# Optimization experiments

Measured on AMD Instinct MI355X. Metric: run time of the kernel, lower is better.

Reference implementation:

```python
import jax, jax.numpy as jnp
import numpy as np

N_ENT = 50000
N_REL = 500
N_EDGE = 800000
H_DIM = 96
BN_EPS = 1e-5


def setup_inputs() -> dict:
    key = jax.random.key(0)
    k1, k2, k3, k4, k5 = jax.random.split(key, 5)
    return {
        "ent_emb": jax.random.normal(k1, (N_ENT, H_DIM), dtype=jnp.float32),
        "rel_emb": jax.random.normal(k2, (N_REL, H_DIM), dtype=jnp.float32),
        "neigh_w": jax.random.normal(k3, (H_DIM, H_DIM), dtype=jnp.float32) * (1.0 / np.sqrt(H_DIM)),
        "bn_gamma": jnp.ones((H_DIM,), dtype=jnp.float32),
        "bn_beta": jnp.zeros((H_DIM,), dtype=jnp.float32),
        "rel_id": jax.random.randint(k4, (N_EDGE,), 0, N_REL, dtype=jnp.int64),
        "dst": jax.random.randint(k5, (N_EDGE,), 0, N_ENT, dtype=jnp.int64),
    }


def reference(ent_emb, rel_emb, neigh_w, bn_gamma, bn_beta, rel_id, dst):
    n_nodes = ent_emb.shape[0]
    # per-edge gather: edge feature = relation embedding  [E, D]
    e = rel_emb[rel_id]
    # e_dot_v: dot of edge feature with destination node embedding  [E]
    score = jnp.sum(e * ent_emb[dst], axis=-1)
    # edge softmax over incoming edges of each destination node
    seg_max = jax.ops.segment_max(score, dst, num_segments=n_nodes)  # [N]
    w = jnp.exp(score - seg_max[dst])                                # [E]
    seg_sum = jax.ops.segment_sum(w, dst, num_segments=n_nodes)      # [N]
    alpha = w / seg_sum[dst]                                         # [E]
    # weighted scatter-sum aggregation into destination nodes  [N, D]
    neigh = jax.ops.segment_sum(e * alpha[:, None], dst, num_segments=n_nodes)
    # linear
    out = neigh @ neigh_w
    # BatchNorm1d (training mode: batch stats over nodes, biased var)
    mu = jnp.mean(out, axis=0)
    var = jnp.mean((out - mu) ** 2, axis=0)
    out = (out - mu) * jax.lax.rsqrt(var + BN_EPS) * bn_gamma + bn_beta
    return jnp.tanh(out)
```

## Files before the change

### kernel.cpp

```cpp
#include <hip/hip_runtime.h>
#include <math.h>

#define N_ENT   50000
#define N_REL   500
#define N_EDGE  800000
#define H       96
#define BN_EPS  1e-5f
#define DEG_CAP 48

#define BUCKET_BLOCKS ((N_EDGE + 255) / 256)
#define RELW_BLOCKS   ((N_REL * H + 255) / 256)

__global__ __launch_bounds__(256) void k_bucket_relw(
        const int* __restrict__ dst, const int* __restrict__ rel_id,
        int* __restrict__ cursor, unsigned short* __restrict__ pay,
        const float* __restrict__ rel, const float* __restrict__ W,
        float* __restrict__ relW) {
    if (blockIdx.x < BUCKET_BLOCKS) {
        int e = blockIdx.x * 256 + threadIdx.x;
        if (e >= N_EDGE) return;
        int d = dst[e];
        int r = rel_id[e];
        int p = atomicAdd(cursor + d, 1);
        if (p < DEG_CAP) pay[d * DEG_CAP + p] = (unsigned short)r;
    } else {
        int t = (blockIdx.x - BUCKET_BLOCKS) * 256 + threadIdx.x;
        if (t >= N_REL * H) return;
        int r = t / H;
        int c = t - r * H;
        const float* rr = rel + (size_t)r * H;
        const float* wc = W + c;
        float acc = 0.0f;
#pragma unroll 4
        for (int k = 0; k < H; ++k)
            acc += rr[k] * wc[(size_t)k * H];
        relW[t] = acc;
    }
}

__global__ __launch_bounds__(256) void k_node(
        const float* __restrict__ ent, const float* __restrict__ rel,
        const unsigned short* __restrict__ pay, const int* __restrict__ cursor,
        const float* __restrict__ relW, float* __restrict__ out) {
    __shared__ float sh_w[4][DEG_CAP];
    __shared__ int   sh_r[4][DEG_CAP];
    int wv   = threadIdx.x >> 6;
    int lane = threadIdx.x & 63;
    int n = blockIdx.x * 4 + wv;
    if (n >= N_ENT) return;
    int cnt = min(cursor[n], DEG_CAP);

    {
        int q  = lane & 3;
        int jj = lane >> 2;
        const float4* er = (const float4*)(ent + (size_t)n * H) + q * 6;
        float4 e0 = er[0], e1 = er[1], e2 = er[2], e3 = er[3], e4 = er[4], e5 = er[5];
        int npass = (cnt + 15) >> 4;
        for (int p = 0; p < npass; ++p) {
            int j = (p << 4) + jj;
            bool valid = (j < cnt);
            int rid = valid ? (int)pay[n * DEG_CAP + j] : 0;
            float part = 0.0f;
            if (valid) {
                const float4* rr = (const float4*)(rel + (size_t)rid * H) + q * 6;
                float4 b;
                b = rr[0]; part += e0.x*b.x + e0.y*b.y + e0.z*b.z + e0.w*b.w;
                b = rr[1]; part += e1.x*b.x + e1.y*b.y + e1.z*b.z + e1.w*b.w;
                b = rr[2]; part += e2.x*b.x + e2.y*b.y + e2.z*b.z + e2.w*b.w;
                b = rr[3]; part += e3.x*b.x + e3.y*b.y + e3.z*b.z + e3.w*b.w;
                b = rr[4]; part += e4.x*b.x + e4.y*b.y + e4.z*b.z + e4.w*b.w;
                b = rr[5]; part += e5.x*b.x + e5.y*b.y + e5.z*b.z + e5.w*b.w;
            }
            part += __shfl_xor(part, 1);
            part += __shfl_xor(part, 2);
            if (valid && q == 0) { sh_w[wv][j] = part; sh_r[wv][j] = rid; }
        }
    }

    {
        float sc = (lane < cnt) ? sh_w[wv][lane] : -INFINITY;
        float m = sc;
#pragma unroll
        for (int off = 1; off < 64; off <<= 1)
            m = fmaxf(m, __shfl_xor(m, off));
        float w = (lane < cnt) ? __expf(sc - m) : 0.0f;
        float s = w;
#pragma unroll
        for (int off = 1; off < 64; off <<= 1)
            s += __shfl_xor(s, off);
        float inv = (cnt > 0) ? 1.0f / s : 0.0f;
        if (lane < cnt) sh_w[wv][lane] = w * inv;
    }

    int es = (lane >= 24) ? 1 : 0;
    int g  = lane - es * 24;
    float4 acc = make_float4(0.f, 0.f, 0.f, 0.f);
    if (lane < 48) {
        for (int k = es; k < cnt; k += 2) {
            float w  = sh_w[wv][k];
            int rid  = sh_r[wv][k];
            float4 f = ((const float4*)(relW + (size_t)rid * H))[g];
            acc.x += w * f.x; acc.y += w * f.y;
            acc.z += w * f.z; acc.w += w * f.w;
        }
    }
    float ox = __shfl(acc.x, lane + 24);
    float oy = __shfl(acc.y, lane + 24);
    float oz = __shfl(acc.z, lane + 24);
    float ow = __shfl(acc.w, lane + 24);
    if (lane < 24) {
        float4 o = make_float4(acc.x + ox, acc.y + oy, acc.z + oz, acc.w + ow);
        ((float4*)(out + (size_t)n * H))[lane] = o;
    }
}

__global__ __launch_bounds__(256) void k_bnstats(
        const float* __restrict__ out, float* __restrict__ bn_sum,
        float* __restrict__ bn_sumsq) {
    __shared__ float sh_s[4][H], sh_q[4][H];
    int wave = threadIdx.x >> 6;
    int lane = threadIdx.x & 63;
    float4 s = make_float4(0.f, 0.f, 0.f, 0.f);
    float4 ss = make_float4(0.f, 0.f, 0.f, 0.f);
    if (lane < H / 4) {
        for (int n = blockIdx.x * 4 + wave; n < N_ENT; n += gridDim.x * 4) {
            float4 v = ((const float4*)(out + (size_t)n * H))[lane];
            s.x += v.x; s.y += v.y; s.z += v.z; s.w += v.w;
            ss.x += v.x * v.x; ss.y += v.y * v.y;
            ss.z += v.z * v.z; ss.w += v.w * v.w;
        }
        ((float4*)sh_s[wave])[lane] = s;
        ((float4*)sh_q[wave])[lane] = ss;
    }
    __syncthreads();
    int d = threadIdx.x;
    if (d < H) {
        float ts = sh_s[0][d] + sh_s[1][d] + sh_s[2][d] + sh_s[3][d];
        float tq = sh_q[0][d] + sh_q[1][d] + sh_q[2][d] + sh_q[3][d];
        atomicAdd(bn_sum + d, ts);
        atomicAdd(bn_sumsq + d, tq);
    }
}

__device__ __forceinline__ float fast_tanh(float x) {
    return 1.0f - 2.0f / (__expf(2.0f * x) + 1.0f);
}

__global__ __launch_bounds__(256) void k_bnapply(
        float* __restrict__ out, const float* __restrict__ bn_sum,
        const float* __restrict__ bn_sumsq, const float* __restrict__ gamma,
        const float* __restrict__ beta) {
    int t = blockIdx.x * 256 + threadIdx.x;
    if (t >= N_ENT * H / 4) return;
    int c4 = t % (H / 4);
    const float inv_n = 1.0f / (float)N_ENT;
    float4 v = ((const float4*)out)[t];
    float4 sm = ((const float4*)bn_sum)[c4];
    float4 sq = ((const float4*)bn_sumsq)[c4];
    float4 g  = ((const float4*)gamma)[c4];
    float4 b  = ((const float4*)beta)[c4];
    float mu0 = sm.x * inv_n, mu1 = sm.y * inv_n, mu2 = sm.z * inv_n, mu3 = sm.w * inv_n;
    float r0 = rsqrtf(sq.x * inv_n - mu0 * mu0 + BN_EPS);
    float r1 = rsqrtf(sq.y * inv_n - mu1 * mu1 + BN_EPS);
    float r2 = rsqrtf(sq.z * inv_n - mu2 * mu2 + BN_EPS);
    float r3 = rsqrtf(sq.w * inv_n - mu3 * mu3 + BN_EPS);
    float4 o;
    o.x = fast_tanh((v.x - mu0) * r0 * g.x + b.x);
    o.y = fast_tanh((v.y - mu1) * r1 * g.y + b.y);
    o.z = fast_tanh((v.z - mu2) * r2 * g.z + b.z);
    o.w = fast_tanh((v.w - mu3) * r3 * g.w + b.w);
    ((float4*)out)[t] = o;
}

extern "C" void kernel_launch(void* const* d_in, const int* in_sizes, int n_in,
                              void* d_out, int out_size, void* d_ws, size_t ws_size,
                              hipStream_t stream) {
    const float* ent   = (const float*)d_in[0];
    const float* rel   = (const float*)d_in[1];
    const float* W     = (const float*)d_in[2];
    const float* gamma = (const float*)d_in[3];
    const float* beta  = (const float*)d_in[4];
    const int* rel_id  = (const int*)d_in[5];
    const int* dst     = (const int*)d_in[6];
    float* out = (float*)d_out;

    float* ws       = (float*)d_ws;
    int*   cursor   = (int*)ws;
    float* bn_sum   = ws + N_ENT;
    float* bn_sumsq = bn_sum + H;
    float* relW     = bn_sumsq + H;
    unsigned short* pay = (unsigned short*)(relW + N_REL * H);

    hipMemsetAsync(cursor, 0, (size_t)(N_ENT + 2 * H) * sizeof(int), stream);

    k_bucket_relw<<<BUCKET_BLOCKS + RELW_BLOCKS, 256, 0, stream>>>(
        dst, rel_id, cursor, pay, rel, W, relW);
    k_node<<<(N_ENT + 3) / 4, 256, 0, stream>>>(ent, rel, pay, cursor, relW, out);
    k_bnstats<<<784, 256, 0, stream>>>(out, bn_sum, bn_sumsq);
    k_bnapply<<<(N_ENT * H / 4 + 255) / 256, 256, 0, stream>>>(
        out, bn_sum, bn_sumsq, gamma, beta);
}
```

Measured before the change: 208.9 us.

## Fuse BN statistics into node kernel and pack relation ids into 10-bit slots

Batch-norm sum and sum-of-squares are now accumulated inside the node kernel from the freshly computed rows, striped across 64 partial buffers to spread atomic contention, and reduced by a tiny single-block kernel. This removes the separate pass that re-read the whole output. Relation ids are packed three per 32-bit word with atomicOr, which requires zeroing the payload buffer in the memset. The memset gets larger and every edge insertion now costs an extra atomic.

```diff
diff --git a/kernel.cpp b/kernel.cpp
--- a/kernel.cpp
+++ b/kernel.cpp
@@ -7,13 +7,15 @@
 #define H       96
 #define BN_EPS  1e-5f
 #define DEG_CAP 48
+#define WPB     16
+#define NSTRIPE 64
 
 #define BUCKET_BLOCKS ((N_EDGE + 255) / 256)
 #define RELW_BLOCKS   ((N_REL * H + 255) / 256)
 
 __global__ __launch_bounds__(256) void k_bucket_relw(
         const int* __restrict__ dst, const int* __restrict__ rel_id,
-        int* __restrict__ cursor, unsigned short* __restrict__ pay,
+        int* __restrict__ cursor, unsigned* __restrict__ pay,
         const float* __restrict__ rel, const float* __restrict__ W,
         float* __restrict__ relW) {
     if (blockIdx.x < BUCKET_BLOCKS) {
@@ -21,8 +23,12 @@
         if (e >= N_EDGE) return;
         int d = dst[e];
         int r = rel_id[e];
-        int p = atomicAdd(cursor + d, 1);
-        if (p < DEG_CAP) pay[d * DEG_CAP + p] = (unsigned short)r;
+        int pos = atomicAdd(cursor + d, 1);
+        if (pos < DEG_CAP) {
+            int w = pos / 3;
+            int s = (pos - w * 3) * 10;
+            atomicOr(pay + d * WPB + w, (unsigned)r << s);
+        }
     } else {
         int t = (blockIdx.x - BUCKET_BLOCKS) * 256 + threadIdx.x;
         if (t >= N_REL * H) return;
@@ -40,14 +46,15 @@
 
 __global__ __launch_bounds__(256) void k_node(
         const float* __restrict__ ent, const float* __restrict__ rel,
-        const unsigned short* __restrict__ pay, const int* __restrict__ cursor,
-        const float* __restrict__ relW, float* __restrict__ out) {
+        const unsigned* __restrict__ pay, const int* __restrict__ cursor,
+        const float* __restrict__ relW, float* __restrict__ out,
+        float* __restrict__ bn_parts) {
     __shared__ float sh_w[4][DEG_CAP];
     __shared__ int   sh_r[4][DEG_CAP];
+    __shared__ float sh_s[4][H], sh_q[4][H];
     int wv   = threadIdx.x >> 6;
     int lane = threadIdx.x & 63;
     int n = blockIdx.x * 4 + wv;
-    if (n >= N_ENT) return;
     int cnt = min(cursor[n], DEG_CAP);
 
     {
@@ -59,7 +66,12 @@
         for (int p = 0; p < npass; ++p) {
             int j = (p << 4) + jj;
             bool valid = (j < cnt);
-            int rid = valid ? (int)pay[n * DEG_CAP + j] : 0;
+            int rid = 0;
+            if (valid) {
+                int wi = j / 3;
+                unsigned wq = pay[n * WPB + wi];
+                rid = (int)((wq >> ((j - wi * 3) * 10)) & 1023u);
+            }
             float part = 0.0f;
             if (valid) {
                 const float4* rr = (const float4*)(rel + (size_t)rid * H) + q * 6;
@@ -111,35 +123,31 @@
     if (lane < 24) {
         float4 o = make_float4(acc.x + ox, acc.y + oy, acc.z + oz, acc.w + ow);
         ((float4*)(out + (size_t)n * H))[lane] = o;
-    }
-}
-
-__global__ __launch_bounds__(256) void k_bnstats(
-        const float* __restrict__ out, float* __restrict__ bn_sum,
-        float* __restrict__ bn_sumsq) {
-    __shared__ float sh_s[4][H], sh_q[4][H];
-    int wave = threadIdx.x >> 6;
-    int lane = threadIdx.x & 63;
-    float4 s = make_float4(0.f, 0.f, 0.f, 0.f);
-    float4 ss = make_float4(0.f, 0.f, 0.f, 0.f);
-    if (lane < H / 4) {
-        for (int n = blockIdx.x * 4 + wave; n < N_ENT; n += gridDim.x * 4) {
-            float4 v = ((const float4*)(out + (size_t)n * H))[lane];
-            s.x += v.x; s.y += v.y; s.z += v.z; s.w += v.w;
-            ss.x += v.x * v.x; ss.y += v.y * v.y;
-            ss.z += v.z * v.z; ss.w += v.w * v.w;
-        }
-        ((float4*)sh_s[wave])[lane] = s;
-        ((float4*)sh_q[wave])[lane] = ss;
-    }
+        float4 sq = make_float4(o.x * o.x, o.y * o.y, o.z * o.z, o.w * o.w);
+        ((float4*)sh_s[wv])[lane] = o;
+        ((float4*)sh_q[wv])[lane] = sq;
+    }
+
     __syncthreads();
     int d = threadIdx.x;
+    float* part = bn_parts + (size_t)(blockIdx.x & (NSTRIPE - 1)) * (2 * H);
     if (d < H) {
-        float ts = sh_s[0][d] + sh_s[1][d] + sh_s[2][d] + sh_s[3][d];
-        float tq = sh_q[0][d] + sh_q[1][d] + sh_q[2][d] + sh_q[3][d];
-        atomicAdd(bn_sum + d, ts);
-        atomicAdd(bn_sumsq + d, tq);
-    }
+        atomicAdd(part + d, sh_s[0][d] + sh_s[1][d] + sh_s[2][d] + sh_s[3][d]);
+    } else if (d < 2 * H) {
+        int dd = d - H;
+        atomicAdd(part + H + dd,
+                  sh_q[0][dd] + sh_q[1][dd] + sh_q[2][dd] + sh_q[3][dd]);
+    }
+}
+
+__global__ __launch_bounds__(192) void k_bnreduce(
+        const float* __restrict__ bn_parts, float* __restrict__ bn_stats) {
+    int d = threadIdx.x;
+    float s = 0.0f;
+#pragma unroll
+    for (int c = 0; c < NSTRIPE; ++c)
+        s += bn_parts[(size_t)c * (2 * H) + d];
+    bn_stats[d] = s;
 }
 
 __device__ __forceinline__ float fast_tanh(float x) {
@@ -147,16 +155,15 @@
 }
 
 __global__ __launch_bounds__(256) void k_bnapply(
-        float* __restrict__ out, const float* __restrict__ bn_sum,
-        const float* __restrict__ bn_sumsq, const float* __restrict__ gamma,
-        const float* __restrict__ beta) {
+        float* __restrict__ out, const float* __restrict__ bn_stats,
+        const float* __restrict__ gamma, const float* __restrict__ beta) {
     int t = blockIdx.x * 256 + threadIdx.x;
     if (t >= N_ENT * H / 4) return;
     int c4 = t % (H / 4);
     const float inv_n = 1.0f / (float)N_ENT;
     float4 v = ((const float4*)out)[t];
-    float4 sm = ((const float4*)bn_sum)[c4];
-    float4 sq = ((const float4*)bn_sumsq)[c4];
+    float4 sm = ((const float4*)bn_stats)[c4];
+    float4 sq = ((const float4*)(bn_stats + H))[c4];
     float4 g  = ((const float4*)gamma)[c4];
     float4 b  = ((const float4*)beta)[c4];
     float mu0 = sm.x * inv_n, mu1 = sm.y * inv_n, mu2 = sm.z * inv_n, mu3 = sm.w * inv_n;
@@ -184,19 +191,21 @@
     const int* dst     = (const int*)d_in[6];
     float* out = (float*)d_out;
 
-    float* ws       = (float*)d_ws;
-    int*   cursor   = (int*)ws;
-    float* bn_sum   = ws + N_ENT;
-    float* bn_sumsq = bn_sum + H;
-    float* relW     = bn_sumsq + H;
-    unsigned short* pay = (unsigned short*)(relW + N_REL * H);
-
-    hipMemsetAsync(cursor, 0, (size_t)(N_ENT + 2 * H) * sizeof(int), stream);
+    float*    ws       = (float*)d_ws;
+    int*      cursor   = (int*)ws;
+    float*    bn_parts = ws + N_ENT;
+    unsigned* pay      = (unsigned*)(ws + N_ENT + NSTRIPE * 2 * H);
+    float*    relW     = ws + N_ENT + NSTRIPE * 2 * H + N_ENT * WPB;
+    float*    bn_stats = relW + N_REL * H;
+
+    const size_t zwords = (size_t)N_ENT + NSTRIPE * 2 * H + (size_t)N_ENT * WPB;
+    hipMemsetAsync(cursor, 0, zwords * sizeof(int), stream);
 
     k_bucket_relw<<<BUCKET_BLOCKS + RELW_BLOCKS, 256, 0, stream>>>(
         dst, rel_id, cursor, pay, rel, W, relW);
-    k_node<<<(N_ENT + 3) / 4, 256, 0, stream>>>(ent, rel, pay, cursor, relW, out);
-    k_bnstats<<<784, 256, 0, stream>>>(out, bn_sum, bn_sumsq);
+    k_node<<<N_ENT / 4, 256, 0, stream>>>(
+        ent, rel, pay, cursor, relW, out, bn_parts);
+    k_bnreduce<<<1, 192, 0, stream>>>(bn_parts, bn_stats);
     k_bnapply<<<(N_ENT * H / 4 + 255) / 256, 256, 0, stream>>>(
-        out, bn_sum, bn_sumsq, gamma, beta);
-}
+        out, bn_stats, gamma, beta);
+}
```

Measured after the change: 215.2 us. 3.0% more time.
